# Performance work log

Measured on AMD Instinct MI355X. Metric: run time of the kernel, lower is better.

The kernel has to match this reference:

```python
import jax, jax.numpy as jnp
import numpy as np
from jax import lax

B, S, V, D, L = 16, 512, 32000, 512, 64


def setup_inputs() -> dict:
    key = jax.random.key(0)
    ks = jax.random.split(key, 6)
    return {
        "token_ids": jax.random.randint(ks[0], (B, S), 0, V),
        "vocab_emb": jax.random.normal(ks[1], (V, D), jnp.float32) * 0.02,
        "pos_W": jax.random.normal(ks[2], (D, L), jnp.float32) * (1.0 / np.sqrt(D)),
        "pos_b": jnp.zeros((L,), jnp.float32),
        "W1": jax.random.normal(ks[3], (2 * D, D), jnp.float32) * (1.0 / np.sqrt(2 * D)),
        "b1": jnp.zeros((D,), jnp.float32),
        "w2": jax.random.normal(ks[4], (D,), jnp.float32) * (1.0 / np.sqrt(D)),
        "b2": jnp.zeros((), jnp.float32),
    }


def reference(token_ids, vocab_emb, pos_W, pos_b, W1, b1, w2, b2):
    feats = vocab_emb[token_ids]                      # (B, S, D) embedding lookup
    logits = feats @ pos_W + pos_b                    # (B, S, L) POS-tag logits
    cls = jnp.argmax(logits, axis=-1)                 # (B, S)

    # same_cls_as_neighbor: sequence-chain neighbors OR same predicted class, no self loops
    idx = jnp.arange(S)
    chain = jnp.abs(idx[:, None] - idx[None, :]) == 1
    not_self = idx[:, None] != idx[None, :]
    same = cls[:, :, None] == cls[:, None, :]
    adj = (chain[None] | same) & not_self[None]       # (B, S, S) bool

    # rnn_linear (2D->D) followed directly by rnn_linear2 (D->1) with no nonlinearity:
    # score(i,j) = w2.(W1a f_i + W1b f_j + b1) + b2 = f_i.u + f_j.v + c  (exact rewrite)
    W1a, W1b = W1[:D], W1[D:]
    u = W1a @ w2
    v = W1b @ w2
    c = b1 @ w2 + b2

    def parse_one(f, a):
        # greedy easy-first merge loop: S-1 merges until one node remains
        def step(carry, _):
            f, a, tot = carry
            si = f @ u                                 # (S,)
            sj = f @ v                                 # (S,)
            sc = jnp.where(a, si[:, None] + sj[None, :] + c, -jnp.inf)  # (S, S)
            k = jnp.argmax(sc)                         # flat argmax over neighbor pairs
            i, j = k // S, k % S
            best = sc.reshape(-1)[k]
            parent = f[i] @ W1a + f[j] @ W1b + b1      # parent feature of merged pair
            f = f.at[i].set(parent)                    # slot i <- parent
            row = a[i] | a[j]                          # parent inherits both neighborhoods
            a = a.at[i, :].set(row).at[:, i].set(row)
            a = a.at[j, :].set(False).at[:, j].set(False)  # slot j removed
            a = a.at[i, i].set(False)
            return (f, a, tot + best), jnp.stack([i, j])

        (_, _, tot), tree = lax.scan(step, (f, a, jnp.float32(0.0)), None, length=S - 1)
        return tot, tree

    total_score, parse_tree = jax.vmap(parse_one)(feats, adj)
    return total_score, parse_tree                    # (B,), (B, S-1, 2)
```

## Files before the change

### kernel.cpp

```cpp
#include <hip/hip_runtime.h>

#define cB 16
#define cS 512
#define cD 512
#define cL 64
#define cG 8
#define cT 1024

constexpr size_t FCOPY   = (size_t)cB * cS * cD * 4;
constexpr size_t OFF_F0  = 0;
constexpr size_t OFF_F1  = FCOPY;
constexpr size_t OFF_U   = 2 * FCOPY;
constexpr size_t OFF_V   = OFF_U  + 2048;
constexpr size_t OFF_UA  = OFF_V  + 2048;
constexpr size_t OFF_UB  = OFF_UA + 2048;
constexpr size_t OFF_VA  = OFF_UB + 2048;
constexpr size_t OFF_VB  = OFF_VA + 2048;
constexpr size_t OFF_SC  = OFF_VB + 2048;
constexpr size_t OFF_SI  = OFF_SC + 64;
constexpr size_t OFF_SJ  = OFF_SI + (size_t)cB*cS*4;
constexpr size_t OFF_CLS = OFF_SJ + (size_t)cB*cS*4;
constexpr size_t OFF_ADJ = OFF_CLS+ (size_t)cB*cS*4;
constexpr size_t OFF_RM  = OFF_ADJ+ (size_t)cB*cS*64;
constexpr size_t OFF_RA  = OFF_RM + (size_t)cB*cS*4;
constexpr size_t OFF_BAR = ((OFF_RA + (size_t)cB*cS*4 + 127) & ~(size_t)127);

template <int CTRL, int RMASK>
__device__ __forceinline__ void dpp_max_step(float& v, int& k) {
    const float ov = __int_as_float(__builtin_amdgcn_update_dpp(
        (int)0xff800000u, __float_as_int(v), CTRL, RMASK, 0xf, false));
    const int ok = __builtin_amdgcn_update_dpp(
        0x7fffffff, k, CTRL, RMASK, 0xf, false);
    if (ov > v || (ov == v && ok < k)) { v = ov; k = ok; }
}

__device__ __forceinline__ void wave_max64(float& v, int& k) {
    dpp_max_step<0x111, 0xf>(v, k);
    dpp_max_step<0x112, 0xf>(v, k);
    dpp_max_step<0x114, 0xf>(v, k);
    dpp_max_step<0x118, 0xf>(v, k);
    dpp_max_step<0x142, 0xa>(v, k);
    dpp_max_step<0x143, 0xc>(v, k);
}

template <int N>
__device__ __forceinline__ float dpp_shl_add(float x) {
    const float o = __int_as_float(__builtin_amdgcn_update_dpp(
        0, __float_as_int(x), 0x100 + N , 0xf, 0xf, false));
    return x + o;
}

__device__ __forceinline__ void vk_max(float& v, int& k, float ov, int ok) {
    if (ov > v || (ov == v && ok < k)) { v = ov; k = ok; }
}

__global__ void k1_uvc(const float* __restrict__ W1, const float* __restrict__ b1,
                       const float* __restrict__ w2, const float* __restrict__ b2,
                       char* __restrict__ ws) {
    const int t = threadIdx.x;
    const int r = blockIdx.x;
    if (r == 1025) {
        unsigned* bar = (unsigned*)(ws + OFF_BAR);
        for (int i = t; i < 4096; i += 256) bar[i] = 0u;
        return;
    }
    __shared__ float rs[256];
    float acc;
    if (r < 1024) {
        const float* row = W1 + (size_t)r * cD;
        acc = row[t] * w2[t] + row[t + 256] * w2[t + 256];
    } else {
        acc = b1[t] * w2[t] + b1[t + 256] * w2[t + 256];
    }
    rs[t] = acc; __syncthreads();
    for (int o = 128; o; o >>= 1) { if (t < o) rs[t] += rs[t + o]; __syncthreads(); }
    if (t == 0) {
        if (r < 512)        ((float*)(ws + OFF_U))[r] = rs[0];
        else if (r < 1024)  ((float*)(ws + OFF_V))[r - 512] = rs[0];
        else                ((float*)(ws + OFF_SC))[0] = rs[0] + b2[0];
    }
}

__global__ void k1b_proj(const float* __restrict__ W1, const float* __restrict__ b1,
                         char* __restrict__ ws) {
    __shared__ float ru[256], rv[256];
    const int t = threadIdx.x;
    const int k = blockIdx.x;
    const float* U = (const float*)(ws + OFF_U);
    const float* V = (const float*)(ws + OFF_V);
    const float* row = (k < 1024) ? (W1 + (size_t)k * cD) : b1;
    ru[t] = row[t] * U[t] + row[t + 256] * U[t + 256];
    rv[t] = row[t] * V[t] + row[t + 256] * V[t + 256];
    __syncthreads();
    for (int o = 128; o; o >>= 1) {
        if (t < o) { ru[t] += ru[t + o]; rv[t] += rv[t + o]; }
        __syncthreads();
    }
    if (t == 0) {
        if (k < 512)       { ((float*)(ws + OFF_UA))[k] = ru[0]; ((float*)(ws + OFF_VA))[k] = rv[0]; }
        else if (k < 1024) { ((float*)(ws + OFF_UB))[k - 512] = ru[0]; ((float*)(ws + OFF_VB))[k - 512] = rv[0]; }
        else               { ((float*)(ws + OFF_SC))[1] = ru[0]; ((float*)(ws + OFF_SC))[2] = rv[0]; }
    }
}

__global__ void k2_feat(const int* __restrict__ tok, const float* __restrict__ emb,
                        char* __restrict__ ws) {
    __shared__ float ru[256], rv[256];
    const int t = threadIdx.x;
    const int bs = blockIdx.x;
    const float* U = (const float*)(ws + OFF_U);
    const float* V = (const float*)(ws + OFF_V);
    float* F = (float*)(ws + OFF_F0);
    const int tk = tok[bs];
    const float* src = emb + (size_t)tk * cD;
    float* dst = F + (size_t)bs * cD;
    const float e0 = src[t], e1 = src[t + 256];
    dst[t] = e0; dst[t + 256] = e1;
    ru[t] = e0 * U[t] + e1 * U[t + 256];
    rv[t] = e0 * V[t] + e1 * V[t + 256];
    __syncthreads();
    for (int o = 128; o; o >>= 1) {
        if (t < o) { ru[t] += ru[t + o]; rv[t] += rv[t + o]; }
        __syncthreads();
    }
    if (t == 0) {
        ((float*)(ws + OFF_SI))[bs] = ru[0];
        ((float*)(ws + OFF_SJ))[bs] = rv[0];
    }
}

__global__ void k3_cls(const float* __restrict__ posW, const float* __restrict__ posb,
                       char* __restrict__ ws) {
    const int t = threadIdx.x;
    const int bs = blockIdx.x;
    const float* frow = (const float*)(ws + OFF_F0) + (size_t)bs * cD;
    float acc = posb[t];
    for (int k = 0; k < cD; k++) acc += frow[k] * posW[(size_t)k * cL + t];
    int idx = t;
    for (int off = 32; off; off >>= 1) {
        float ov = __shfl_down(acc, off, 64);
        int   oi = __shfl_down(idx, off, 64);
        if (ov > acc || (ov == acc && oi < idx)) { acc = ov; idx = oi; }
    }
    if (t == 0) ((int*)(ws + OFF_CLS))[bs] = idx;
}

__global__ void k4_adj(char* __restrict__ ws) {
    __shared__ float rsv[256]; __shared__ int rsk[256];
    const int t = threadIdx.x;
    const int bs = blockIdx.x;
    const int b = bs >> 9, r = bs & 511;
    const int* cls = (const int*)(ws + OFF_CLS) + (size_t)b * cS;
    const float* SJ = (const float*)(ws + OFF_SJ) + (size_t)b * cS;
    const float sir = ((const float*)(ws + OFF_SI))[bs];
    const float c0 = ((const float*)(ws + OFF_SC))[0];
    unsigned long long* adjrow = (unsigned long long*)(ws + OFF_ADJ) + (size_t)bs * 8;
    const int cr = cls[r];
    float bv = -INFINITY; int bc = 0;
    for (int p = 0; p < 2; p++) {
        const int c = p * 256 + t;
        int dd = c - r; if (dd < 0) dd = -dd;
        const bool allowed = (c != r) && (dd == 1 || cls[c] == cr);
        unsigned long long m = __ballot(allowed);
        if ((t & 63) == 0) adjrow[p * 4 + (t >> 6)] = m;
        if (allowed) {
            float val = sir + SJ[c] + c0;
            if (val > bv || (val == bv && c < bc)) { bv = val; bc = c; }
        }
    }
    rsv[t] = bv; rsk[t] = bc; __syncthreads();
    for (int o = 128; o; o >>= 1) {
        if (t < o) {
            float s2 = rsv[t + o]; int k2 = rsk[t + o];
            if (s2 > rsv[t] || (s2 == rsv[t] && k2 < rsk[t])) { rsv[t] = s2; rsk[t] = k2; }
        }
        __syncthreads();
    }
    if (t == 0) { ((float*)(ws + OFF_RM))[bs] = rsv[0]; ((int*)(ws + OFF_RA))[bs] = rsk[0]; }
}

__global__ void __launch_bounds__(cT, 4)
parse_main(const float* __restrict__ W1, const float* __restrict__ b1,
           char* __restrict__ ws, float* __restrict__ out) {
    const int t  = threadIdx.x;
    const int b  = blockIdx.x & 15;
    const int g  = blockIdx.x >> 4;
    const int d0 = g * 64;
    const int wf = t >> 6;
    const int ln = t & 63;
    const int wv = wf >> 1;
    const int h  = wf & 1;

    unsigned long long* F64[2] = {
        (unsigned long long*)(ws + OFF_F0) + (size_t)b * cS * cD / 2,
        (unsigned long long*)(ws + OFF_F1) + (size_t)b * cS * cD / 2 };
    unsigned* prog = (unsigned*)(ws + OFF_BAR) + (size_t)b * 256;
    const float* SCp = (const float*)(ws + OFF_SC);
    const float c0 = SCp[0], cu_c = SCp[1], cv_c = SCp[2];

    __shared__ unsigned long long AdjL[8 * 512];
    __shared__ float SIl[512], SJl[512], rmax[512];
    __shared__ int   rarg[512];
    __shared__ int   tp[512];
    __shared__ float rsh[1024];
    __shared__ float ws_si[8], ws_sj[8];
    __shared__ int   s_info;
    __shared__ int   rescanList[516]; __shared__ int nresc;
    __shared__ int   iterLog[512];

    const int kbase = wv * 128;
    float2 wreg2[32];
#pragma unroll
    for (int m = 0; m < 32; m++) {
        wreg2[m].x = W1[(size_t)(kbase + 4 * m + 2 * h)     * cD + d0 + ln];
        wreg2[m].y = W1[(size_t)(kbase + 4 * m + 2 * h + 1) * cD + d0 + ln];
    }

    const int xk = (wv & 3) * 128 + 2 * ln;
    float cu0 = 0.f, cu1 = 0.f, cv0 = 0.f, cv1 = 0.f;
    if (h == 0) {
        const float* cu_base = (const float*)(ws + ((wv < 4) ? OFF_UA : OFF_UB));
        const float* cvb     = (const float*)(ws + ((wv < 4) ? OFF_VA : OFF_VB));
        cu0 = cu_base[xk]; cu1 = cu_base[xk + 1];
        cv0 = cvb[xk];     cv1 = cvb[xk + 1];
    }

    if (t < cS) {
        SIl[t]  = ((const float*)(ws + OFF_SI))[b * cS + t];
        SJl[t]  = ((const float*)(ws + OFF_SJ))[b * cS + t];
        rmax[t] = ((const float*)(ws + OFF_RM))[b * cS + t];
        rarg[t] = ((const int*)(ws + OFF_RA))[b * cS + t];
        tp[t]   = -2;
        const unsigned long long* AG =
            (const unsigned long long*)(ws + OFF_ADJ) + (size_t)b * cS * 8;
#pragma unroll
        for (int wq = 0; wq < 8; wq++) AdjL[wq * 512 + t] = AG[(size_t)t * 8 + wq];
    }
    float b1v = 0.f;
    if (wf == 15) b1v = b1[d0 + ln];
    bool myAlive = true;
    float tot = 0.f;
    int minp = 0;
    if (t == 0) nresc = 0;
    __syncthreads();

    for (int it = 0; it < cS - 1; ++it) {
        if (wf == 0) {
            float v0[8]; int k0[8];
#pragma unroll
            for (int k = 0; k < 8; k++) {
                const int r = k * 64 + ln;
                v0[k] = rmax[r];
                k0[k] = (r << 9) | (rarg[r] & 511);
            }
            vk_max(v0[0], k0[0], v0[1], k0[1]);
            vk_max(v0[2], k0[2], v0[3], k0[3]);
            vk_max(v0[4], k0[4], v0[5], k0[5]);
            vk_max(v0[6], k0[6], v0[7], k0[7]);
            vk_max(v0[0], k0[0], v0[2], k0[2]);
            vk_max(v0[4], k0[4], v0[6], k0[6]);
            vk_max(v0[0], k0[0], v0[4], k0[4]);
            float bv = v0[0]; int bk = k0[0];
            wave_max64(bv, bk);
            const int bk63 = __builtin_amdgcn_readlane(bk, 63);
            const int pbi = bk63 >> 9, pbj = bk63 & 511;
            if (ln == 0) {
                const int info0 = pbi | (pbj << 9);
                s_info = info0;
                iterLog[it] = info0;
                nresc = 0;
                if (g == 0) {
                    tot += __int_as_float(
                        __builtin_amdgcn_readlane(__float_as_int(bv), 63));
                }
            }
        }
        __syncthreads();
        const int info = s_info;
        const int bi = info & 511, bj = (info >> 9) & 511;

        const int myrow = (wv < 4) ? bi : bj;
        const int tpr   = tp[myrow];
        const int mypar = tpr & 1;
        const int need  = (tpr >> 1) + 1;
        int pari = 0;
        if (wf == 15) pari = tp[bi] & 1;
        if (need > minp) {
            const int gq = 2 * (wv & 3);
            const unsigned un = (unsigned)need;
            for (;;) {
                unsigned v = 0xffffffffu;
                if (ln < 2) v = __hip_atomic_load(prog + (gq + ln) * 32, __ATOMIC_RELAXED,
                                                  __HIP_MEMORY_SCOPE_AGENT);
                if (__ballot(v >= un) == ~0ull) break;
                __builtin_amdgcn_s_sleep(1);
            }
            minp = need;
        }
        unsigned long long xv = __hip_atomic_load(
            F64[mypar] + (size_t)myrow * 256 + (wv & 3) * 64 + ln,
            __ATOMIC_RELAXED, __HIP_MEMORY_SCOPE_AGENT);
        float2 f2; __builtin_memcpy(&f2, &xv, 8);
        if (h == 0) {
            float csi = f2.x * cu0 + f2.y * cu1;
            float csj = f2.x * cv0 + f2.y * cv1;
            csi += __shfl_down(csi, 32, 64);  csj += __shfl_down(csj, 32, 64);
            csi += __shfl_down(csi, 16, 64);  csj += __shfl_down(csj, 16, 64);
            csi = dpp_shl_add<8>(csi);  csj = dpp_shl_add<8>(csj);
            csi = dpp_shl_add<4>(csi);  csj = dpp_shl_add<4>(csj);
            csi = dpp_shl_add<2>(csi);  csj = dpp_shl_add<2>(csj);
            csi = dpp_shl_add<1>(csi);  csj = dpp_shl_add<1>(csj);
            if (ln == 0) { ws_si[wv] = csi; ws_sj[wv] = csj; }
        }
        {
            const int ix = __float_as_int(f2.x), iy = __float_as_int(f2.y);
            float aP = 0.f, aQ = 0.f;
            if (h == 0) {
#pragma unroll
                for (int m = 0; m < 32; m++) {
                    const float q0 = __int_as_float(__builtin_amdgcn_readlane(ix, 2 * m));
                    const float q1 = __int_as_float(__builtin_amdgcn_readlane(iy, 2 * m));
                    aP = fmaf(wreg2[m].x, q0, aP);
                    aQ = fmaf(wreg2[m].y, q1, aQ);
                }
            } else {
#pragma unroll
                for (int m = 0; m < 32; m++) {
                    const float q0 = __int_as_float(__builtin_amdgcn_readlane(ix, 2 * m + 1));
                    const float q1 = __int_as_float(__builtin_amdgcn_readlane(iy, 2 * m + 1));
                    aP = fmaf(wreg2[m].x, q0, aP);
                    aQ = fmaf(wreg2[m].y, q1, aQ);
                }
            }
            rsh[t] = aP + aQ;
        }
        __syncthreads();

        if (wf == 15) {
            float p = b1v;
#pragma unroll
            for (int q = 0; q < 8; q++)
                p += rsh[(2 * q) * 64 + ln] + rsh[(2 * q + 1) * 64 + ln];
            __hip_atomic_store((float*)F64[pari ^ 1] + (size_t)bi * 512 + d0 + ln, p,
                               __ATOMIC_RELAXED, __HIP_MEMORY_SCOPE_AGENT);
            asm volatile("s_waitcnt vmcnt(0)" ::: "memory");
            if (ln == 0)
                __hip_atomic_store(prog + g * 32, (unsigned)(it + 1), __ATOMIC_RELAXED,
                                   __HIP_MEMORY_SCOPE_AGENT);
        } else if (wf == 8) {
            if (ln < 8) {
                const int wq = ln;
                const int wbi = bi >> 6, wbj = bj >> 6;
                const unsigned long long mbi = 1ull << (bi & 63), mbj = 1ull << (bj & 63);
                unsigned long long nw = AdjL[wq * 512 + bi] | AdjL[wq * 512 + bj];
                if (wq == wbi) nw &= ~mbi;
                if (wq == wbj) nw &= ~mbj;
                AdjL[wq * 512 + bi] = nw;
            }
        } else if (t < cS) {
            float su = (ln < 8) ? ws_si[ln] : 0.f;
            float sv = (ln < 8) ? ws_sj[ln] : 0.f;
            su = dpp_shl_add<4>(su);  sv = dpp_shl_add<4>(sv);
            su = dpp_shl_add<2>(su);  sv = dpp_shl_add<2>(sv);
            su = dpp_shl_add<1>(su);  sv = dpp_shl_add<1>(sv);
            const float sn = __int_as_float(
                __builtin_amdgcn_readfirstlane(__float_as_int(su))) + cu_c;
            const float jn = __int_as_float(
                __builtin_amdgcn_readfirstlane(__float_as_int(sv))) + cv_c;

            const float sjn_ = jn;
            const int wbi = bi >> 6, wbj = bj >> 6;
            const unsigned long long mbi = 1ull << (bi & 63), mbj = 1ull << (bj & 63);
            const int r = t;
            if (r == bj) {
                if (myAlive) { myAlive = false; rmax[t] = -INFINITY; }
            } else if (r == bi) {
                int slot = atomicAdd(&nresc, 1); rescanList[slot] = bi;
                SIl[bi] = sn; SJl[bi] = jn;
                tp[bi] = (it << 1) | ((tp[bi] & 1) ^ 1);
            } else if (myAlive) {
                unsigned long long wi = AdjL[wbi * 512 + r];
                unsigned long long wj = (wbj == wbi) ? wi : AdjL[wbj * 512 + r];
                const bool nb = ((wi & mbi) | (wj & mbj)) != 0ull;
                if (wbi == wbj) {
                    AdjL[wbi * 512 + r] = (wi & ~(mbi | mbj)) | (nb ? mbi : 0ull);
                } else {
                    AdjL[wbi * 512 + r] = (wi & ~mbi) | (nb ? mbi : 0ull);
                    AdjL[wbj * 512 + r] = wj & ~mbj;
                }
                const int ra = rarg[t];
                if (ra == bi || ra == bj) {
                    int slot = atomicAdd(&nresc, 1); rescanList[slot] = r;
                } else if (nb) {
                    const float val = SIl[r] + sjn_ + c0;
                    if (val > rmax[t] || (val == rmax[t] && bi < ra)) { rmax[t] = val; rarg[t] = bi; }
                }
            }
        }
        __syncthreads();

        const int nr = nresc;
        for (int q = wf; q < nr; q += 16) {
            const int r = rescanList[q];
            const float sir = SIl[r];
            float bv2 = -INFINITY; int bc2 = 0x7fffffff;
#pragma unroll
            for (int k = 0; k < 8; k++) {
                const unsigned long long word = AdjL[k * 512 + r];
                if ((word >> ln) & 1ull) {
                    const int c = k * 64 + ln;
                    const float val = sir + SJl[c] + c0;
                    if (val > bv2 || (val == bv2 && c < bc2)) { bv2 = val; bc2 = c; }
                }
            }
            wave_max64(bv2, bc2);
            if (ln == 63) { rmax[r] = bv2; rarg[r] = bc2; }
        }
        __syncthreads();
    }

    __syncthreads();
    if (g == 0) {
        if (t < 2 * (cS - 1)) {
            const int e = iterLog[t >> 1];
            const int val = (t & 1) ? ((e >> 9) & 511) : (e & 511);
            out[16 + b * 1022 + t] = (float)val;
        }
        if (t == 0) out[b] = tot;
    }
}

extern "C" void kernel_launch(void* const* d_in, const int* in_sizes, int n_in,
                              void* d_out, int out_size, void* d_ws, size_t ws_size,
                              hipStream_t stream) {
    const int*   token_ids = (const int*)d_in[0];
    const float* vocab_emb = (const float*)d_in[1];
    const float* pos_W     = (const float*)d_in[2];
    const float* pos_b     = (const float*)d_in[3];
    const float* W1        = (const float*)d_in[4];
    const float* b1        = (const float*)d_in[5];
    const float* w2        = (const float*)d_in[6];
    const float* b2        = (const float*)d_in[7];
    float* out = (float*)d_out;
    char*  ws  = (char*)d_ws;

    k1_uvc<<<1026, 256, 0, stream>>>(W1, b1, w2, b2, ws);
    k1b_proj<<<1025, 256, 0, stream>>>(W1, b1, ws);
    k2_feat<<<cB * cS, 256, 0, stream>>>(token_ids, vocab_emb, ws);
    k3_cls<<<cB * cS, 64, 0, stream>>>(pos_W, pos_b, ws);
    k4_adj<<<cB * cS, 256, 0, stream>>>(ws);

    void* args[] = { (void*)&W1, (void*)&b1, (void*)&ws, (void*)&out };
    hipLaunchCooperativeKernel((void*)parse_main, dim3(cB * cG), dim3(cT),
                               args, 0, stream);
}
```

Measured before the change: 2.690 ms.

## Drop the post-rescan barrier by routing rescan results through side buffers

Waves 1-15 now do the per-row rescans and write results into side buffers (sideV/sideK), then bump a workgroup-scoped atomic counter instead of meeting at a trailing __syncthreads. Wave 0 spin-waits on that counter and folds the pending side results into its next argmax selection. Rows still waiting on a rescan are marked with a pending bit in rarg, and the update phase copies their side values back into rmax/rarg. This removes one full-workgroup barrier from each of the 511 merge iterations. In exchange it adds spin-wait traffic, extra LDS bookkeeping, and subtle ordering risks around the pending flags and the double-buffered rescan counters.

New measurement: 2.802 ms. +4.2%, slower.

```diff
diff --git a/kernel.cpp b/kernel.cpp
--- a/kernel.cpp
+++ b/kernel.cpp
@@ -6,6 +6,8 @@
 #define cL 64
 #define cG 8
 #define cT 1024
+
+#define PENDB (1 << 30)
 
 constexpr size_t FCOPY   = (size_t)cB * cS * cD * 4;
 constexpr size_t OFF_F0  = 0;
@@ -205,7 +207,10 @@
     __shared__ float rsh[1024];
     __shared__ float ws_si[8], ws_sj[8];
     __shared__ int   s_info;
-    __shared__ int   rescanList[516]; __shared__ int nresc;
+    __shared__ int   rescanList[516];
+    __shared__ int   nrescBuf[2];
+    __shared__ float sideV[512]; __shared__ int sideK[512];
+    __shared__ int   rjoin;
     __shared__ int   iterLog[512];
 
     const int kbase = wv * 128;
@@ -229,7 +234,7 @@
         SIl[t]  = ((const float*)(ws + OFF_SI))[b * cS + t];
         SJl[t]  = ((const float*)(ws + OFF_SJ))[b * cS + t];
         rmax[t] = ((const float*)(ws + OFF_RM))[b * cS + t];
-        rarg[t] = ((const int*)(ws + OFF_RA))[b * cS + t];
+        rarg[t] = ((const int*)(ws + OFF_RA))[b * cS + t] & ~PENDB;
         tp[t]   = -2;
         const unsigned long long* AG =
             (const unsigned long long*)(ws + OFF_ADJ) + (size_t)b * cS * 8;
@@ -241,17 +246,19 @@
     bool myAlive = true;
     float tot = 0.f;
     int minp = 0;
-    if (t == 0) nresc = 0;
+    if (t == 0) { nrescBuf[0] = 0; nrescBuf[1] = 0; rjoin = 0; }
     __syncthreads();
 
     for (int it = 0; it < cS - 1; ++it) {
         if (wf == 0) {
+            const int nr_prev = (it > 0) ? nrescBuf[(it - 1) & 1] : 0;
             float v0[8]; int k0[8];
 #pragma unroll
             for (int k = 0; k < 8; k++) {
                 const int r = k * 64 + ln;
-                v0[k] = rmax[r];
-                k0[k] = (r << 9) | (rarg[r] & 511);
+                const int ra = rarg[r];
+                v0[k] = (ra & PENDB) ? -INFINITY : rmax[r];
+                k0[k] = (r << 9) | (ra & 511);
             }
             vk_max(v0[0], k0[0], v0[1], k0[1]);
             vk_max(v0[2], k0[2], v0[3], k0[3]);
@@ -261,6 +268,18 @@
             vk_max(v0[4], k0[4], v0[6], k0[6]);
             vk_max(v0[0], k0[0], v0[4], k0[4]);
             float bv = v0[0]; int bk = k0[0];
+            if (it > 0) {
+                const int target = 15 * it;
+                while (__hip_atomic_load(&rjoin, __ATOMIC_ACQUIRE,
+                                         __HIP_MEMORY_SCOPE_WORKGROUP) < target) {}
+                for (int base = 0; base < nr_prev; base += 64) {
+                    const int q = base + ln;
+                    if (q < nr_prev) {
+                        const int r2 = rescanList[q];
+                        vk_max(bv, bk, sideV[r2], (r2 << 9) | (sideK[r2] & 511));
+                    }
+                }
+            }
             wave_max64(bv, bk);
             const int bk63 = __builtin_amdgcn_readlane(bk, 63);
             const int pbi = bk63 >> 9, pbj = bk63 & 511;
@@ -268,7 +287,7 @@
                 const int info0 = pbi | (pbj << 9);
                 s_info = info0;
                 iterLog[it] = info0;
-                nresc = 0;
+                nrescBuf[it & 1] = 0;
                 if (g == 0) {
                     tot += __int_as_float(
                         __builtin_amdgcn_readlane(__float_as_int(bv), 63));
@@ -368,16 +387,24 @@
             const float jn = __int_as_float(
                 __builtin_amdgcn_readfirstlane(__float_as_int(sv))) + cv_c;
 
+            const int r = t;
+            {
+                const int ra0 = rarg[r];
+                if (ra0 & PENDB) {
+                    rmax[r] = sideV[r];
+                    rarg[r] = sideK[r] & ~PENDB;
+                }
+            }
             const float sjn_ = jn;
             const int wbi = bi >> 6, wbj = bj >> 6;
             const unsigned long long mbi = 1ull << (bi & 63), mbj = 1ull << (bj & 63);
-            const int r = t;
             if (r == bj) {
                 if (myAlive) { myAlive = false; rmax[t] = -INFINITY; }
             } else if (r == bi) {
-                int slot = atomicAdd(&nresc, 1); rescanList[slot] = bi;
+                int slot = atomicAdd(&nrescBuf[it & 1], 1); rescanList[slot] = bi;
                 SIl[bi] = sn; SJl[bi] = jn;
                 tp[bi] = (it << 1) | ((tp[bi] & 1) ^ 1);
+                rarg[bi] |= PENDB;
             } else if (myAlive) {
                 unsigned long long wi = AdjL[wbi * 512 + r];
                 unsigned long long wj = (wbj == wbi) ? wi : AdjL[wbj * 512 + r];
@@ -390,7 +417,8 @@
                 }
                 const int ra = rarg[t];
                 if (ra == bi || ra == bj) {
-                    int slot = atomicAdd(&nresc, 1); rescanList[slot] = r;
+                    int slot = atomicAdd(&nrescBuf[it & 1], 1); rescanList[slot] = r;
+                    rarg[t] = ra | PENDB;
                 } else if (nb) {
                     const float val = SIl[r] + sjn_ + c0;
                     if (val > rmax[t] || (val == rmax[t] && bi < ra)) { rmax[t] = val; rarg[t] = bi; }
@@ -399,24 +427,28 @@
         }
         __syncthreads();
 
-        const int nr = nresc;
-        for (int q = wf; q < nr; q += 16) {
-            const int r = rescanList[q];
-            const float sir = SIl[r];
-            float bv2 = -INFINITY; int bc2 = 0x7fffffff;
-#pragma unroll
-            for (int k = 0; k < 8; k++) {
-                const unsigned long long word = AdjL[k * 512 + r];
-                if ((word >> ln) & 1ull) {
-                    const int c = k * 64 + ln;
-                    const float val = sir + SJl[c] + c0;
-                    if (val > bv2 || (val == bv2 && c < bc2)) { bv2 = val; bc2 = c; }
-                }
-            }
-            wave_max64(bv2, bc2);
-            if (ln == 63) { rmax[r] = bv2; rarg[r] = bc2; }
-        }
-        __syncthreads();
+        if (wf > 0) {
+            const int nr = nrescBuf[it & 1];
+            for (int q = wf - 1; q < nr; q += 15) {
+                const int r = rescanList[q];
+                const float sir = SIl[r];
+                float bv2 = -INFINITY; int bc2 = 0x7fffffff;
+#pragma unroll
+                for (int k = 0; k < 8; k++) {
+                    const unsigned long long word = AdjL[k * 512 + r];
+                    if ((word >> ln) & 1ull) {
+                        const int c = k * 64 + ln;
+                        const float val = sir + SJl[c] + c0;
+                        if (val > bv2 || (val == bv2 && c < bc2)) { bv2 = val; bc2 = c; }
+                    }
+                }
+                wave_max64(bv2, bc2);
+                if (ln == 63) { sideV[r] = bv2; sideK[r] = bc2; }
+            }
+            if (ln == 0)
+                __hip_atomic_fetch_add(&rjoin, 1, __ATOMIC_RELEASE,
+                                       __HIP_MEMORY_SCOPE_WORKGROUP);
+        }
     }
 
     __syncthreads();
```
